# Kernel optimization log

Hardware: AMD Instinct MI355X
Metric: run time of the kernel (lower is better)

The kernel has to match this reference:

```python
import jax, jax.numpy as jnp
import numpy as np

N, H, E, K, C, M = 4096, 512, 512, 64, 128, 4  # tokens, hidden, embed, categories, children/cat, max_num_children
IN = E + H  # LSTMCell input size


def setup_inputs() -> dict:
    key = jax.random.key(0)
    ks = jax.random.split(key, 12)
    s = 0.05
    return {
        "et": jax.random.normal(ks[0], (N, H), jnp.float32),
        "x": jax.random.normal(ks[1], (N, IN), jnp.float32),
        "h": jax.random.normal(ks[2], (N, H), jnp.float32),
        "c": jax.random.normal(ks[3], (N, H), jnp.float32),
        "cat": jax.random.randint(ks[4], (N,), 0, K, jnp.int32),
        "ci": jax.random.randint(ks[5], (N,), 0, M, jnp.int32),
        # per-category prediction Linear(hidden_size -> |children(category)|)
        "W_lin": jax.random.normal(ks[6], (K, C, H), jnp.float32) * s,
        "b_lin": jax.random.normal(ks[7], (K, C), jnp.float32) * s,
        # per-child-index LSTMCell(embedding+hidden -> hidden), torch gate order i,f,g,o
        "W_ih": jax.random.normal(ks[8], (M, 4 * H, IN), jnp.float32) * s,
        "W_hh": jax.random.normal(ks[9], (M, 4 * H, H), jnp.float32) * s,
        "b_ih": jax.random.normal(ks[10], (M, 4 * H), jnp.float32) * s,
        "b_hh": jax.random.normal(ks[11], (M, 4 * H), jnp.float32) * s,
    }


def reference(et, x, h, c, cat, ci, W_lin, b_lin, W_ih, W_hh, b_ih, b_hh):
    # get_log_odds: route each token to its category's Linear (gather weights, per-token matvec)
    Wg = W_lin[cat]                                   # [N, C, H]
    log_odds = jnp.einsum('nh,nch->nc', et, Wg) + b_lin[cat]  # [N, C]

    # get_next: LSTMCell selected by child_index. Only M=4 cells, so compute all
    # cells' gates densely (efficient GEMMs) and select with a one-hot mix.
    gates_all = (jnp.einsum('ni,kgi->nkg', x, W_ih)
                 + jnp.einsum('nh,kgh->nkg', h, W_hh)
                 + (b_ih + b_hh)[None])               # [N, M, 4H]
    sel = jax.nn.one_hot(ci, M, dtype=gates_all.dtype)  # [N, M]
    gates = jnp.einsum('nkg,nk->ng', gates_all, sel)     # [N, 4H]
    i_, f_, g_, o_ = jnp.split(gates, 4, axis=-1)
    c2 = jax.nn.sigmoid(f_) * c + jax.nn.sigmoid(i_) * jnp.tanh(g_)
    h2 = jax.nn.sigmoid(o_) * jnp.tanh(c2)
    return log_odds, h2, c2
```

## Files before the change

kernel.cpp:

```cpp
#include <hip/hip_runtime.h>
#include <hip/hip_bf16.h>
#include <stdint.h>

#define NTOK 4096
#define HID  512
#define INSZ 1024
#define KIN  1536
#define KCAT 64
#define CCH  128
#define MCELL 4
#define G4H  2048
#define SLOTS 5120

typedef unsigned short u16;
typedef __bf16 bf16x8 __attribute__((ext_vector_type(8)));
typedef float  f32x4  __attribute__((ext_vector_type(4)));

__device__ __forceinline__ u16 f2bf(float f) {
    unsigned u = __float_as_uint(f);
    u += 0x7fffu + ((u >> 16) & 1u);
    return (u16)(u >> 16);
}
__device__ __forceinline__ float bf2f(u16 v) {
    return __uint_as_float(((unsigned)v) << 16);
}
__device__ __forceinline__ void store_bf8(u16* p, float4 a, float4 b) {
    ushort4 r0, r1;
    r0.x = f2bf(a.x); r0.y = f2bf(a.y); r0.z = f2bf(a.z); r0.w = f2bf(a.w);
    r1.x = f2bf(b.x); r1.y = f2bf(b.y); r1.z = f2bf(b.z); r1.w = f2bf(b.w);
    *reinterpret_cast<ushort4*>(p) = r0;
    *reinterpret_cast<ushort4*>(p + 4) = r1;
}
__device__ __forceinline__ void gl16(const u16* g, u16* l) {
    __builtin_amdgcn_global_load_lds((const __attribute__((address_space(1))) void*)g,
                                     (__attribute__((address_space(3))) void*)l, 16, 0, 0);
}

#define CH_W  (8192 * 192)
#define CH_L  (8192 * 64)
#define CH_A  (4097 * 192)
#define CH_TOT (CH_W + CH_L + CH_A)
#define PK_BLOCKS 2048

__global__ __launch_bounds__(256) void fat_pack(
    const float* __restrict__ x, const float* __restrict__ h,
    const float* __restrict__ Wih, const float* __restrict__ Whh,
    const float* __restrict__ W_lin,
    const int* __restrict__ ci, const int* __restrict__ cat,
    int* __restrict__ meta, int* __restrict__ perm_ci, int* __restrict__ perm_cat,
    u16* __restrict__ A_tok, u16* __restrict__ Wb, u16* __restrict__ Wlin)
{
    if (blockIdx.x == 0) {
        __shared__ int cnt_ci[MCELL], cur_ci[MCELL];
        __shared__ int cnt_cat[KCAT], cur_cat[KCAT];
        int tid = threadIdx.x;
        if (tid < MCELL) cnt_ci[tid] = 0;
        if (tid < KCAT)  cnt_cat[tid] = 0;
        __syncthreads();
        for (int t = tid; t < NTOK; t += 256) {
            atomicAdd(&cnt_ci[ci[t]], 1);
            atomicAdd(&cnt_cat[cat[t]], 1);
        }
        __syncthreads();
        if (tid == 0) {
            int off = 0;
            for (int m = 0; m < MCELL; ++m) {
                int p = (cnt_ci[m] + 255) & ~255;
                meta[m] = p; meta[4 + m] = off; cur_ci[m] = off; off += p;
            }
            off = 0;
            for (int i = 0; i < 128; ++i) meta[136 + i] = -1;
            for (int k = 0; k < KCAT; ++k) {
                int p = (cnt_cat[k] + 63) & ~63;
                meta[8 + k] = p; meta[72 + k] = off; cur_cat[k] = off;
                for (int i = 0; i < p / 64; ++i) meta[136 + off / 64 + i] = k;
                off += p;
            }
        }
        __syncthreads();
        for (int i = tid; i < SLOTS; i += 256) perm_ci[i] = -1;
        for (int i = tid; i < 8192; i += 256) perm_cat[i] = -1;
        __syncthreads();
        for (int t = tid; t < NTOK; t += 256) {
            perm_ci[atomicAdd(&cur_ci[ci[t]], 1)] = t;
            perm_cat[atomicAdd(&cur_cat[cat[t]], 1)] = t;
        }
        return;
    }
    for (int i = (blockIdx.x - 1) * 256 + threadIdx.x; i < CH_TOT; i += (PK_BLOCKS - 1) * 256) {
        if (i < CH_W) {
            int row = i / 192, cc = i - row * 192;
            int m = row >> 11, j = row & 2047;
            int srow = (j & 3) * HID + (j >> 2);
            int c = cc * 8;
            const float* src = (c < INSZ) ? (Wih + ((size_t)m * G4H + srow) * INSZ + c)
                                          : (Whh + ((size_t)m * G4H + srow) * HID + (c - INSZ));
            store_bf8(Wb + (size_t)row * KIN + c,
                      *(const float4*)src, *(const float4*)(src + 4));
        } else if (i < CH_W + CH_L) {
            int i2 = i - CH_W;
            int row = i2 >> 6, cc = i2 & 63;
            const float* src = W_lin + (size_t)row * HID + cc * 8;
            store_bf8(Wlin + (size_t)row * HID + cc * 8,
                      *(const float4*)src, *(const float4*)(src + 4));
        } else {
            int i3 = i - (CH_W + CH_L);
            int row = i3 / 192, cc = i3 - row * 192;
            int c = cc * 8;
            u16* dst = A_tok + (size_t)row * KIN + c;
            if (row == NTOK) {
                *reinterpret_cast<int4*>(dst) = make_int4(0, 0, 0, 0);
            } else {
                const float* src = (c < INSZ) ? (x + (size_t)row * INSZ + c)
                                              : (h + (size_t)row * HID + (c - INSZ));
                store_bf8(dst, *(const float4*)src, *(const float4*)(src + 4));
            }
        }
    }
}

__global__ __launch_bounds__(256, 2) void mega_gemm(
    const u16* __restrict__ A_tok,
    const u16* __restrict__ Wb,
    const u16* __restrict__ Wlin,
    const float* __restrict__ et,
    const float* __restrict__ b_lin,
    const float* __restrict__ c,
    const float* __restrict__ b_ih,
    const float* __restrict__ b_hh,
    const int* __restrict__ meta,
    const int* __restrict__ perm_ci,
    const int* __restrict__ perm_cat,
    float* __restrict__ out)
{
    __shared__ __align__(16) u16 As[16384];
    __shared__ __align__(16) u16 Bs[8192];
    __shared__ int sperm[256];

    int tid = threadIdx.x;
    int lane = tid & 63, wave = tid >> 6;
    int qd = lane >> 4, l15 = lane & 15;
    int rsw = l15 & 7;

    int id = blockIdx.x;
    if (id < 640) {
        int g = id & 63;
        int rt = id >> 6;
        int m = g >> 4, ct = g & 15;
        int pcnt = meta[m];
        if (rt * 256 >= pcnt) return;
        int row0 = meta[4 + m] + rt * 256;

        sperm[tid] = perm_ci[row0 + tid];
        __syncthreads();

        const u16* gA[8]; const u16* gB[4];
        u16* lA[8]; u16* lB[4];
        #pragma unroll
        for (int j = 0; j < 8; ++j) {
            int q = j * 256 + wave * 64 + lane;
            int row = q >> 3, kc = (q & 7) ^ (row & 7);
            int t = sperm[row];
            const u16* base = A_tok + (size_t)(t >= 0 ? t : NTOK) * KIN;
            gA[j] = base + kc * 8;
            lA[j] = As + q * 8;
        }
        #pragma unroll
        for (int j = 0; j < 4; ++j) {
            int q = j * 256 + wave * 64 + lane;
            int row = q >> 3, kc = (q & 7) ^ (row & 7);
            gB[j] = Wb + ((size_t)m * G4H + ct * 128 + row) * KIN + kc * 8;
            lB[j] = Bs + q * 8;
        }

        int wm = wave >> 1, wn = wave & 1;

        f32x4 acc[8][4];
        #pragma unroll
        for (int i = 0; i < 8; ++i)
            #pragma unroll
            for (int j = 0; j < 4; ++j)
                acc[i][j] = (f32x4){0.f, 0.f, 0.f, 0.f};

        for (int ks = 0; ks < KIN / 64; ++ks) {
            #pragma unroll
            for (int j = 0; j < 8; ++j) { gl16(gA[j], lA[j]); gA[j] += 64; }
            #pragma unroll
            for (int j = 0; j < 4; ++j) { gl16(gB[j], lB[j]); gB[j] += 64; }
            __syncthreads();
            #pragma unroll
            for (int ks2 = 0; ks2 < 2; ++ks2) {
                int ch = (ks2 * 4 + qd) ^ rsw;
                bf16x8 fb[4];
                #pragma unroll
                for (int tj = 0; tj < 4; ++tj) {
                    int row = wn * 64 + tj * 16 + l15;
                    fb[tj] = *reinterpret_cast<const bf16x8*>(&Bs[row * 64 + ch * 8]);
                }
                #pragma unroll
                for (int ti = 0; ti < 8; ++ti) {
                    int row = wm * 128 + ti * 16 + l15;
                    bf16x8 fa = *reinterpret_cast<const bf16x8*>(&As[row * 64 + ch * 8]);
                    #pragma unroll
                    for (int tj = 0; tj < 4; ++tj)
                        acc[ti][tj] = __builtin_amdgcn_mfma_f32_16x16x32_bf16(fa, fb[tj], acc[ti][tj], 0, 0, 0);
                }
            }
            __syncthreads();
        }

        int gt = l15 & 3;
        float bias[4];
        #pragma unroll
        for (int tj = 0; tj < 4; ++tj) {
            int u = ct * 32 + wn * 16 + tj * 4 + (l15 >> 2);
            bias[tj] = b_ih[m * G4H + gt * HID + u] + b_hh[m * G4H + gt * HID + u];
        }
        int b0 = lane & 1, b1 = lane & 2;
        const size_t o_h2 = (size_t)NTOK * CCH;
        const size_t o_c2 = o_h2 + (size_t)NTOK * HID;
        #pragma unroll
        for (int ti = 0; ti < 8; ++ti) {
            int t = sperm[wm * 128 + ti * 16 + qd * 4 + (lane & 3)];
            #pragma unroll
            for (int tj = 0; tj < 4; ++tj) {
                float v0 = acc[ti][tj][0] + bias[tj];
                float v1 = acc[ti][tj][1] + bias[tj];
                float v2 = acc[ti][tj][2] + bias[tj];
                float v3 = acc[ti][tj][3] + bias[tj];
                float tmp;
                tmp = __shfl_xor(b0 ? v0 : v1, 1); if (b0) v0 = tmp; else v1 = tmp;
                tmp = __shfl_xor(b0 ? v2 : v3, 1); if (b0) v2 = tmp; else v3 = tmp;
                tmp = __shfl_xor(b1 ? v0 : v2, 2); if (b1) v0 = tmp; else v2 = tmp;
                tmp = __shfl_xor(b1 ? v1 : v3, 2); if (b1) v1 = tmp; else v3 = tmp;
                if (t >= 0) {
                    int u = ct * 32 + wn * 16 + tj * 4 + (l15 >> 2);
                    float si = 1.f / (1.f + __expf(-v0));
                    float sf = 1.f / (1.f + __expf(-v1));
                    float tg = tanhf(v2);
                    float so = 1.f / (1.f + __expf(-v3));
                    float cold = c[(size_t)t * HID + u];
                    float c2 = sf * cold + si * tg;
                    float h2 = so * tanhf(c2);
                    out[o_h2 + (size_t)t * HID + u] = h2;
                    out[o_c2 + (size_t)t * HID + u] = c2;
                }
            }
        }
    } else {
        int rtl = id - 640;
        int k = meta[136 + rtl];
        if (k < 0) return;
        int r0 = rtl * 64;

        if (tid < 64) sperm[tid] = perm_cat[r0 + tid];
        __syncthreads();

        int rb = tid >> 3;
        int kc = (tid & 7) ^ (rb & 7);

        const u16* gW[4]; u16* lW[4];
        #pragma unroll
        for (int i = 0; i < 4; ++i) {
            gW[i] = Wlin + ((size_t)k * CCH + i * 32 + rb) * HID + kc * 8;
            lW[i] = As + (i * 256 + wave * 64) * 8;
        }
        int ar = tid >> 2;
        int acp = tid & 3;
        int at = sperm[ar];
        const float* asrc = (at >= 0) ? (et + (size_t)at * HID) : nullptr;

        f32x4 acc[4][2];
        #pragma unroll
        for (int i = 0; i < 4; ++i) {
            acc[i][0] = (f32x4){0.f, 0.f, 0.f, 0.f};
            acc[i][1] = (f32x4){0.f, 0.f, 0.f, 0.f};
        }

        for (int kk = 0; kk < HID; kk += 64) {
            #pragma unroll
            for (int i = 0; i < 4; ++i) { gl16(gW[i], lW[i]); gW[i] += 64; }
            #pragma unroll
            for (int j = 0; j < 2; ++j) {
                int dch = acp * 2 + j;
                int sch = dch ^ (ar & 7);
                u16* dst = &Bs[ar * 64 + dch * 8];
                if (asrc) {
                    const float* s = asrc + kk + sch * 8;
                    store_bf8(dst, *(const float4*)s, *(const float4*)(s + 4));
                } else {
                    *reinterpret_cast<int4*>(dst) = make_int4(0, 0, 0, 0);
                }
            }
            __syncthreads();
            #pragma unroll
            for (int ks2 = 0; ks2 < 2; ++ks2) {
                int ch = (ks2 * 4 + qd) ^ rsw;
                bf16x8 fa[4], fb[2];
                #pragma unroll
                for (int ti = 0; ti < 4; ++ti)
                    fa[ti] = *reinterpret_cast<const bf16x8*>(&Bs[(ti * 16 + l15) * 64 + ch * 8]);
                #pragma unroll
                for (int tj = 0; tj < 2; ++tj)
                    fb[tj] = *reinterpret_cast<const bf16x8*>(&As[(wave * 32 + tj * 16 + l15) * 64 + ch * 8]);
                #pragma unroll
                for (int ti = 0; ti < 4; ++ti)
                    #pragma unroll
                    for (int tj = 0; tj < 2; ++tj)
                        acc[ti][tj] = __builtin_amdgcn_mfma_f32_16x16x32_bf16(fa[ti], fb[tj], acc[ti][tj], 0, 0, 0);
            }
            __syncthreads();
        }

        #pragma unroll
        for (int ti = 0; ti < 4; ++ti) {
            #pragma unroll
            for (int tj = 0; tj < 2; ++tj) {
                int n = wave * 32 + tj * 16 + l15;
                float bias = b_lin[k * CCH + n];
                #pragma unroll
                for (int rr = 0; rr < 4; ++rr) {
                    int row = ti * 16 + qd * 4 + rr;
                    int t = sperm[row];
                    if (t >= 0)
                        out[(size_t)t * CCH + n] = acc[ti][tj][rr] + bias;
                }
            }
        }
    }
}

extern "C" void kernel_launch(void* const* d_in, const int* in_sizes, int n_in,
                              void* d_out, int out_size, void* d_ws, size_t ws_size,
                              hipStream_t stream) {
    const float* et    = (const float*)d_in[0];
    const float* x     = (const float*)d_in[1];
    const float* h     = (const float*)d_in[2];
    const float* c     = (const float*)d_in[3];
    const int*   cat   = (const int*)d_in[4];
    const int*   ci    = (const int*)d_in[5];
    const float* W_lin = (const float*)d_in[6];
    const float* b_lin = (const float*)d_in[7];
    const float* W_ih  = (const float*)d_in[8];
    const float* W_hh  = (const float*)d_in[9];
    const float* b_ih  = (const float*)d_in[10];
    const float* b_hh  = (const float*)d_in[11];
    float* out = (float*)d_out;

    char* ws = (char*)d_ws;
    int* meta     = (int*)ws;
    int* perm_ci  = (int*)(ws + 2048);
    int* perm_cat = (int*)(ws + 22528);
    u16* A_tok    = (u16*)(ws + 55296);
    u16* Wb       = (u16*)(ws + 12641280);
    u16* Wlin     = (u16*)(ws + 37807104);

    fat_pack<<<PK_BLOCKS, 256, 0, stream>>>(x, h, W_ih, W_hh, W_lin, ci, cat,
                                            meta, perm_ci, perm_cat, A_tok, Wb, Wlin);

    mega_gemm<<<640 + 128, 256, 0, stream>>>(A_tok, Wb, Wlin, et, b_lin, c,
                                             b_ih, b_hh, meta, perm_ci, perm_cat, out);
}
```

Baseline: 231.0 us.

## Shrink LSTM GEMM row tile to 128 and double-buffer LDS loads

Token rows per LSTM block drop from 256 to 128, with per-cell padding changed to match. That makes more blocks and wastes less padding on the imbalanced per-cell groups. The K loop now double-buffers A and B tiles in a single 64KB shared array, using partial vmcnt waits and explicit barriers so global-to-LDS loads for the next step overlap MFMA work on the current one. The cost is a higher LDS footprint per block, which may limit occupancy, plus a larger grid whose extra blocks mostly exit early.

```diff
diff --git a/kernel.cpp b/kernel.cpp
--- a/kernel.cpp
+++ b/kernel.cpp
@@ -10,7 +10,7 @@
 #define CCH  128
 #define MCELL 4
 #define G4H  2048
-#define SLOTS 5120
+#define SLOTS 4608
 
 typedef unsigned short u16;
 typedef __bf16 bf16x8 __attribute__((ext_vector_type(8)));
@@ -65,7 +65,7 @@
         if (tid == 0) {
             int off = 0;
             for (int m = 0; m < MCELL; ++m) {
-                int p = (cnt_ci[m] + 255) & ~255;
+                int p = (cnt_ci[m] + 127) & ~127;
                 meta[m] = p; meta[4 + m] = off; cur_ci[m] = off; off += p;
             }
             off = 0;
@@ -119,6 +119,8 @@
     }
 }
 
+#define FENCE() __builtin_amdgcn_sched_barrier(0)
+
 __global__ __launch_bounds__(256, 2) void mega_gemm(
     const u16* __restrict__ A_tok,
     const u16* __restrict__ Wb,
@@ -133,9 +135,8 @@
     const int* __restrict__ perm_cat,
     float* __restrict__ out)
 {
-    __shared__ __align__(16) u16 As[16384];
-    __shared__ __align__(16) u16 Bs[8192];
-    __shared__ int sperm[256];
+    __shared__ __align__(16) u16 S[32768];
+    __shared__ int sperm[128];
 
     int tid = threadIdx.x;
     int lane = tid & 63, wave = tid >> 6;
@@ -143,71 +144,90 @@
     int rsw = l15 & 7;
 
     int id = blockIdx.x;
-    if (id < 640) {
+    if (id < 2048) {
         int g = id & 63;
         int rt = id >> 6;
         int m = g >> 4, ct = g & 15;
         int pcnt = meta[m];
-        if (rt * 256 >= pcnt) return;
-        int row0 = meta[4 + m] + rt * 256;
-
-        sperm[tid] = perm_ci[row0 + tid];
-        __syncthreads();
-
-        const u16* gA[8]; const u16* gB[4];
-        u16* lA[8]; u16* lB[4];
-        #pragma unroll
-        for (int j = 0; j < 8; ++j) {
-            int q = j * 256 + wave * 64 + lane;
+        if (rt * 128 >= pcnt) return;
+        int row0 = meta[4 + m] + rt * 128;
+
+        if (tid < 128) sperm[tid] = perm_ci[row0 + tid];
+        __syncthreads();
+
+        const u16* gA[4]; const u16* gB[4];
+        int qq[4];
+        #pragma unroll
+        for (int j = 0; j < 4; ++j) {
+            int q = j * 256 + tid;
             int row = q >> 3, kc = (q & 7) ^ (row & 7);
             int t = sperm[row];
-            const u16* base = A_tok + (size_t)(t >= 0 ? t : NTOK) * KIN;
-            gA[j] = base + kc * 8;
-            lA[j] = As + q * 8;
-        }
-        #pragma unroll
-        for (int j = 0; j < 4; ++j) {
-            int q = j * 256 + wave * 64 + lane;
-            int row = q >> 3, kc = (q & 7) ^ (row & 7);
+            gA[j] = A_tok + (size_t)(t >= 0 ? t : NTOK) * KIN + kc * 8;
             gB[j] = Wb + ((size_t)m * G4H + ct * 128 + row) * KIN + kc * 8;
-            lB[j] = Bs + q * 8;
+            qq[j] = q * 8;
         }
 
         int wm = wave >> 1, wn = wave & 1;
 
-        f32x4 acc[8][4];
-        #pragma unroll
-        for (int i = 0; i < 8; ++i)
+        f32x4 acc[4][4];
+        #pragma unroll
+        for (int i = 0; i < 4; ++i)
             #pragma unroll
             for (int j = 0; j < 4; ++j)
                 acc[i][j] = (f32x4){0.f, 0.f, 0.f, 0.f};
 
-        for (int ks = 0; ks < KIN / 64; ++ks) {
-            #pragma unroll
-            for (int j = 0; j < 8; ++j) { gl16(gA[j], lA[j]); gA[j] += 64; }
-            #pragma unroll
-            for (int j = 0; j < 4; ++j) { gl16(gB[j], lB[j]); gB[j] += 64; }
-            __syncthreads();
-            #pragma unroll
-            for (int ks2 = 0; ks2 < 2; ++ks2) {
-                int ch = (ks2 * 4 + qd) ^ rsw;
-                bf16x8 fb[4];
-                #pragma unroll
-                for (int tj = 0; tj < 4; ++tj) {
-                    int row = wn * 64 + tj * 16 + l15;
-                    fb[tj] = *reinterpret_cast<const bf16x8*>(&Bs[row * 64 + ch * 8]);
-                }
-                #pragma unroll
-                for (int ti = 0; ti < 8; ++ti) {
-                    int row = wm * 128 + ti * 16 + l15;
-                    bf16x8 fa = *reinterpret_cast<const bf16x8*>(&As[row * 64 + ch * 8]);
-                    #pragma unroll
-                    for (int tj = 0; tj < 4; ++tj)
-                        acc[ti][tj] = __builtin_amdgcn_mfma_f32_16x16x32_bf16(fa, fb[tj], acc[ti][tj], 0, 0, 0);
-                }
-            }
-            __syncthreads();
-        }
+#define STAGE(ABASE, BBASE) do { \
+        _Pragma("unroll") \
+        for (int j = 0; j < 4; ++j) { gl16(gA[j], &S[(ABASE) + qq[j]]); gA[j] += 64; } \
+        _Pragma("unroll") \
+        for (int j = 0; j < 4; ++j) { gl16(gB[j], &S[(BBASE) + qq[j]]); gB[j] += 64; } \
+    } while (0)
+
+#define GEMM_STEP(ABASE, BBASE) do { \
+        _Pragma("unroll") \
+        for (int ks2 = 0; ks2 < 2; ++ks2) { \
+            int ch = (ks2 * 4 + qd) ^ rsw; \
+            bf16x8 fb[4]; \
+            _Pragma("unroll") \
+            for (int tj = 0; tj < 4; ++tj) \
+                fb[tj] = *reinterpret_cast<const bf16x8*>(&S[(BBASE) + (wn * 64 + tj * 16 + l15) * 64 + ch * 8]); \
+            _Pragma("unroll") \
+            for (int ti = 0; ti < 4; ++ti) { \
+                bf16x8 fa = *reinterpret_cast<const bf16x8*>(&S[(ABASE) + (wm * 64 + ti * 16 + l15) * 64 + ch * 8]); \
+                _Pragma("unroll") \
+                for (int tj = 0; tj < 4; ++tj) \
+                    acc[ti][tj] = __builtin_amdgcn_mfma_f32_16x16x32_bf16(fa, fb[tj], acc[ti][tj], 0, 0, 0); \
+            } \
+        } \
+    } while (0)
+
+        STAGE(0, 16384);
+        for (int ks = 0; ks < 24; ks += 2) {
+            STAGE(8192, 24576);
+            asm volatile("s_waitcnt vmcnt(8)" ::: "memory");
+            FENCE();
+            __builtin_amdgcn_s_barrier();
+            FENCE();
+            GEMM_STEP(0, 16384);
+            FENCE();
+            __builtin_amdgcn_s_barrier();
+            FENCE();
+            if (ks + 2 < 24) {
+                STAGE(0, 16384);
+                asm volatile("s_waitcnt vmcnt(8)" ::: "memory");
+            } else {
+                asm volatile("s_waitcnt vmcnt(0)" ::: "memory");
+            }
+            FENCE();
+            __builtin_amdgcn_s_barrier();
+            FENCE();
+            GEMM_STEP(8192, 24576);
+            FENCE();
+            __builtin_amdgcn_s_barrier();
+            FENCE();
+        }
+#undef STAGE
+#undef GEMM_STEP
 
         int gt = l15 & 3;
         float bias[4];
@@ -220,8 +240,8 @@
         const size_t o_h2 = (size_t)NTOK * CCH;
         const size_t o_c2 = o_h2 + (size_t)NTOK * HID;
         #pragma unroll
-        for (int ti = 0; ti < 8; ++ti) {
-            int t = sperm[wm * 128 + ti * 16 + qd * 4 + (lane & 3)];
+        for (int ti = 0; ti < 4; ++ti) {
+            int t = sperm[wm * 64 + ti * 16 + qd * 4 + (lane & 3)];
             #pragma unroll
             for (int tj = 0; tj < 4; ++tj) {
                 float v0 = acc[ti][tj][0] + bias[tj];
@@ -248,7 +268,9 @@
             }
         }
     } else {
-        int rtl = id - 640;
+        u16* As = S;
+        u16* Bs = S + 8192;
+        int rtl = id - 2048;
         int k = meta[136 + rtl];
         if (k < 0) return;
         int r0 = rtl * 64;
@@ -358,6 +380,6 @@
     fat_pack<<<PK_BLOCKS, 256, 0, stream>>>(x, h, W_ih, W_hh, W_lin, ci, cat,
                                             meta, perm_ci, perm_cat, A_tok, Wb, Wlin);
 
-    mega_gemm<<<640 + 128, 256, 0, stream>>>(A_tok, Wb, Wlin, et, b_lin, c,
-                                             b_ih, b_hh, meta, perm_ci, perm_cat, out);
-}
+    mega_gemm<<<2048 + 128, 256, 0, stream>>>(A_tok, Wb, Wlin, et, b_lin, c,
+                                              b_ih, b_hh, meta, perm_ci, perm_cat, out);
+}
```

Measured after the change: 232.1 us. About the same (+0.5%).

## Shrink LSTM GEMM row tile to 192, raise occupancy, parallelize metadata scan

Applied to the files above, without the earlier changes.

The LSTM GEMM tile drops from 256 to 192 token rows. The shared A and B buffers are merged into one array sized for three resident blocks per CU, and the launch is resized to match. Padding each cell's group to 192 instead of 256 cuts wasted rows and adds blocks for better load balance across CUs. The serial single-thread prefix computation in the pack kernel is replaced by a parallel scan. In exchange, each B tile gets less reuse per block and register pressure tightens under the 3-block launch bound.

```diff
diff --git a/kernel.cpp b/kernel.cpp
--- a/kernel.cpp
+++ b/kernel.cpp
@@ -10,7 +10,7 @@
 #define CCH  128
 #define MCELL 4
 #define G4H  2048
-#define SLOTS 5120
+#define SLOTS 4992
 
 typedef unsigned short u16;
 typedef __bf16 bf16x8 __attribute__((ext_vector_type(8)));
@@ -53,6 +53,7 @@
     if (blockIdx.x == 0) {
         __shared__ int cnt_ci[MCELL], cur_ci[MCELL];
         __shared__ int cnt_cat[KCAT], cur_cat[KCAT];
+        __shared__ int scan_cat[KCAT];
         int tid = threadIdx.x;
         if (tid < MCELL) cnt_ci[tid] = 0;
         if (tid < KCAT)  cnt_cat[tid] = 0;
@@ -62,20 +63,27 @@
             atomicAdd(&cnt_cat[cat[t]], 1);
         }
         __syncthreads();
-        if (tid == 0) {
+        for (int i = tid; i < 128; i += 256) meta[136 + i] = -1;
+        if (tid < MCELL) {
             int off = 0;
-            for (int m = 0; m < MCELL; ++m) {
-                int p = (cnt_ci[m] + 255) & ~255;
-                meta[m] = p; meta[4 + m] = off; cur_ci[m] = off; off += p;
-            }
-            off = 0;
-            for (int i = 0; i < 128; ++i) meta[136 + i] = -1;
-            for (int k = 0; k < KCAT; ++k) {
-                int p = (cnt_cat[k] + 63) & ~63;
-                meta[8 + k] = p; meta[72 + k] = off; cur_cat[k] = off;
-                for (int i = 0; i < p / 64; ++i) meta[136 + off / 64 + i] = k;
-                off += p;
-            }
+            for (int i = 0; i < tid; ++i) off += (cnt_ci[i] + 191) / 192 * 192;
+            int p = (cnt_ci[tid] + 191) / 192 * 192;
+            meta[tid] = p; meta[4 + tid] = off; cur_ci[tid] = off;
+        }
+        if (tid < KCAT) scan_cat[tid] = (cnt_cat[tid] + 63) & ~63;
+        __syncthreads();
+        for (int d = 1; d < KCAT; d <<= 1) {
+            int v = 0;
+            if (tid < KCAT && tid >= d) v = scan_cat[tid - d];
+            __syncthreads();
+            if (tid < KCAT) scan_cat[tid] += v;
+            __syncthreads();
+        }
+        if (tid < KCAT) {
+            int p = (cnt_cat[tid] + 63) & ~63;
+            int off = scan_cat[tid] - p;
+            meta[8 + tid] = p; meta[72 + tid] = off; cur_cat[tid] = off;
+            for (int i = 0; i < p / 64; ++i) meta[136 + off / 64 + i] = tid;
         }
         __syncthreads();
         for (int i = tid; i < SLOTS; i += 256) perm_ci[i] = -1;
@@ -119,7 +127,7 @@
     }
 }
 
-__global__ __launch_bounds__(256, 2) void mega_gemm(
+__global__ __launch_bounds__(256, 3) void mega_gemm(
     const u16* __restrict__ A_tok,
     const u16* __restrict__ Wb,
     const u16* __restrict__ Wlin,
@@ -133,9 +141,8 @@
     const int* __restrict__ perm_cat,
     float* __restrict__ out)
 {
-    __shared__ __align__(16) u16 As[16384];
-    __shared__ __align__(16) u16 Bs[8192];
-    __shared__ int sperm[256];
+    __shared__ __align__(16) u16 S[20480];
+    __shared__ int sperm[192];
 
     int tid = threadIdx.x;
     int lane = tid & 63, wave = tid >> 6;
@@ -143,48 +150,47 @@
     int rsw = l15 & 7;
 
     int id = blockIdx.x;
-    if (id < 640) {
+    if (id < 1408) {
         int g = id & 63;
         int rt = id >> 6;
         int m = g >> 4, ct = g & 15;
         int pcnt = meta[m];
-        if (rt * 256 >= pcnt) return;
-        int row0 = meta[4 + m] + rt * 256;
-
-        sperm[tid] = perm_ci[row0 + tid];
-        __syncthreads();
-
-        const u16* gA[8]; const u16* gB[4];
-        u16* lA[8]; u16* lB[4];
-        #pragma unroll
-        for (int j = 0; j < 8; ++j) {
-            int q = j * 256 + wave * 64 + lane;
+        if (rt * 192 >= pcnt) return;
+        int row0 = meta[4 + m] + rt * 192;
+
+        if (tid < 192) sperm[tid] = perm_ci[row0 + tid];
+        __syncthreads();
+
+        const u16* gA[6]; const u16* gB[4];
+        u16* lA[6]; u16* lB[4];
+        #pragma unroll
+        for (int j = 0; j < 6; ++j) {
+            int q = j * 256 + tid;
             int row = q >> 3, kc = (q & 7) ^ (row & 7);
             int t = sperm[row];
-            const u16* base = A_tok + (size_t)(t >= 0 ? t : NTOK) * KIN;
-            gA[j] = base + kc * 8;
-            lA[j] = As + q * 8;
+            gA[j] = A_tok + (size_t)(t >= 0 ? t : NTOK) * KIN + kc * 8;
+            lA[j] = &S[q * 8];
         }
         #pragma unroll
         for (int j = 0; j < 4; ++j) {
-            int q = j * 256 + wave * 64 + lane;
+            int q = j * 256 + tid;
             int row = q >> 3, kc = (q & 7) ^ (row & 7);
             gB[j] = Wb + ((size_t)m * G4H + ct * 128 + row) * KIN + kc * 8;
-            lB[j] = Bs + q * 8;
+            lB[j] = &S[12288 + q * 8];
         }
 
         int wm = wave >> 1, wn = wave & 1;
 
-        f32x4 acc[8][4];
-        #pragma unroll
-        for (int i = 0; i < 8; ++i)
+        f32x4 acc[6][4];
+        #pragma unroll
+        for (int i = 0; i < 6; ++i)
             #pragma unroll
             for (int j = 0; j < 4; ++j)
                 acc[i][j] = (f32x4){0.f, 0.f, 0.f, 0.f};
 
         for (int ks = 0; ks < KIN / 64; ++ks) {
             #pragma unroll
-            for (int j = 0; j < 8; ++j) { gl16(gA[j], lA[j]); gA[j] += 64; }
+            for (int j = 0; j < 6; ++j) { gl16(gA[j], lA[j]); gA[j] += 64; }
             #pragma unroll
             for (int j = 0; j < 4; ++j) { gl16(gB[j], lB[j]); gB[j] += 64; }
             __syncthreads();
@@ -195,12 +201,12 @@
                 #pragma unroll
                 for (int tj = 0; tj < 4; ++tj) {
                     int row = wn * 64 + tj * 16 + l15;
-                    fb[tj] = *reinterpret_cast<const bf16x8*>(&Bs[row * 64 + ch * 8]);
-                }
-                #pragma unroll
-                for (int ti = 0; ti < 8; ++ti) {
-                    int row = wm * 128 + ti * 16 + l15;
-                    bf16x8 fa = *reinterpret_cast<const bf16x8*>(&As[row * 64 + ch * 8]);
+                    fb[tj] = *reinterpret_cast<const bf16x8*>(&S[12288 + row * 64 + ch * 8]);
+                }
+                #pragma unroll
+                for (int ti = 0; ti < 6; ++ti) {
+                    int row = wm * 96 + ti * 16 + l15;
+                    bf16x8 fa = *reinterpret_cast<const bf16x8*>(&S[row * 64 + ch * 8]);
                     #pragma unroll
                     for (int tj = 0; tj < 4; ++tj)
                         acc[ti][tj] = __builtin_amdgcn_mfma_f32_16x16x32_bf16(fa, fb[tj], acc[ti][tj], 0, 0, 0);
@@ -220,8 +226,8 @@
         const size_t o_h2 = (size_t)NTOK * CCH;
         const size_t o_c2 = o_h2 + (size_t)NTOK * HID;
         #pragma unroll
-        for (int ti = 0; ti < 8; ++ti) {
-            int t = sperm[wm * 128 + ti * 16 + qd * 4 + (lane & 3)];
+        for (int ti = 0; ti < 6; ++ti) {
+            int t = sperm[wm * 96 + ti * 16 + qd * 4 + (lane & 3)];
             #pragma unroll
             for (int tj = 0; tj < 4; ++tj) {
                 float v0 = acc[ti][tj][0] + bias[tj];
@@ -248,7 +254,9 @@
             }
         }
     } else {
-        int rtl = id - 640;
+        u16* As = S;
+        u16* Bs = S + 8192;
+        int rtl = id - 1408;
         int k = meta[136 + rtl];
         if (k < 0) return;
         int r0 = rtl * 64;
@@ -358,6 +366,6 @@
     fat_pack<<<PK_BLOCKS, 256, 0, stream>>>(x, h, W_ih, W_hh, W_lin, ci, cat,
                                             meta, perm_ci, perm_cat, A_tok, Wb, Wlin);
 
-    mega_gemm<<<640 + 128, 256, 0, stream>>>(A_tok, Wb, Wlin, et, b_lin, c,
-                                             b_ih, b_hh, meta, perm_ci, perm_cat, out);
-}
+    mega_gemm<<<1408 + 128, 256, 0, stream>>>(A_tok, Wb, Wlin, et, b_lin, c,
+                                              b_ih, b_hh, meta, perm_ci, perm_cat, out);
+}
```

Measured after the change: 220.7 us. 4.4% less time.
